# Kernel tuning notes

Hardware: AMD Instinct MI355X
Metric: run time of the kernel (lower is better)

Reference implementation:

```python
import jax, jax.numpy as jnp
import numpy as np

ALPHA = 1.0
EPS = 1e-09
N_PATCH = 128


def _triplet_loss(xp, xn, alpha, eps):
    # xp, xn: [B, N, D], assumed L2-normalized rows
    n = xp.shape[1]
    p_dist = 2.0 - 2.0 * jnp.einsum('bnd,bmd->bnm', xp, xp)   # [B,N,N]
    pn_dist = 2.0 - 2.0 * jnp.einsum('bnd,bmd->bnm', xp, xn)  # [B,N,N]
    # ppn_dist[b,i,j,k] = alpha + p_dist[b,i,j] - pn_dist[b,i,k]
    ppn = alpha + p_dist[:, :, :, None] - pn_dist[:, :, None, :]  # [B,N,N,N]
    mask = ppn <= 0
    pos = jnp.where(mask, 0.0, ppn)
    num = jnp.sum(pos, axis=-1)                                # [B,N,N]
    den = n - jnp.sum(mask, axis=-1).astype(pos.dtype) + eps   # [B,N,N]
    return jnp.mean(num / den)


def setup_inputs() -> dict:
    key = jax.random.key(0)
    latent = jax.random.normal(key, (8192, 512), dtype=jnp.float32)
    return {"latent": latent}


def reference(latent):
    bsz = latent.shape[0] // (2 * N_PATCH)
    latent = latent / jnp.linalg.norm(latent, axis=-1, keepdims=True)
    latent = latent.reshape(bsz, 2, N_PATCH, -1)
    t_latent, c_latent = latent[:, 0], latent[:, 1]
    loss = _triplet_loss(t_latent, c_latent, ALPHA, EPS) + _triplet_loss(c_latent, t_latent, ALPHA, EPS)
    return loss
```

## Files before the change

kernel.cpp:

```cpp
#include <hip/hip_runtime.h>
#include <hip/hip_bf16.h>

constexpr int   D      = 512;
constexpr float ALPHA  = 1.0f;
constexpr float EPS    = 1e-9f;
constexpr float INV_CNT = 1.0f / (32.0f * 128.0f * 128.0f);

constexpr size_t NRM_OFF  = 0;
constexpr size_t PART_OFF = 8388608;

typedef short bf16x8 __attribute__((ext_vector_type(8)));
typedef float f32x4  __attribute__((ext_vector_type(4)));

__device__ __forceinline__ short f2bf(float f) {
    unsigned u = __builtin_bit_cast(unsigned, f);
    unsigned r = (u + 0x7FFFu + ((u >> 16) & 1u)) >> 16;
    return (short)r;
}

typedef __attribute__((address_space(3))) char lds_char;
typedef const __attribute__((address_space(1))) char g_char;
__device__ __forceinline__ void glds16(const void* g, void* l) {
    __builtin_amdgcn_global_load_lds((g_char*)g, (lds_char*)l, 16, 0, 0);
}


__global__ __launch_bounds__(256) void k_normalize(const float* __restrict__ in,
                                                   short* __restrict__ nrm2) {
    const int wid  = threadIdx.x >> 6;
    const int lane = threadIdx.x & 63;
    const int p    = blockIdx.x;
    const int r    = (p & 7) * 1024 + (p >> 3) * 4 + wid;
    const int b    = r >> 8;
    const int row  = r & 255;
    const float4* src = (const float4*)(in + (size_t)r * D);
    float4 x0 = src[2 * lane];
    float4 x1 = src[2 * lane + 1];
    float ss = x0.x*x0.x + x0.y*x0.y + x0.z*x0.z + x0.w*x0.w
             + x1.x*x1.x + x1.y*x1.y + x1.z*x1.z + x1.w*x1.w;
    #pragma unroll
    for (int o = 32; o > 0; o >>= 1) ss += __shfl_xor(ss, o, 64);
    const float inv = rsqrtf(ss);
    bf16x8 v;
    v[0] = f2bf(x0.x * inv); v[1] = f2bf(x0.y * inv);
    v[2] = f2bf(x0.z * inv); v[3] = f2bf(x0.w * inv);
    v[4] = f2bf(x1.x * inv); v[5] = f2bf(x1.y * inv);
    v[6] = f2bf(x1.z * inv); v[7] = f2bf(x1.w * inv);
    const int ks   = lane >> 2;
    const int slot = ((lane & 3) + (row >> 1)) & 3;
    char* dst = (char*)nrm2 + ((((size_t)b * 16 + ks) * 256 + row) * 64 + slot * 16);
    *(bf16x8*)dst = v;
}

constexpr int PSTR = 260;

__global__ __launch_bounds__(256, 4) void k_fused(const short* __restrict__ nrm2,
                                                  float* __restrict__ part) {
    __shared__ __align__(16) char smem[32832];

    const int p     = blockIdx.x;
    const int slot  = p >> 3;
    const int b     = (p & 7) * 4 + (slot & 3);
    const int rem   = slot >> 2;
    const int chunk = rem & 7;
    const int half  = rem >> 3;
    const int w     = threadIdx.x >> 6;
    const int lane  = threadIdx.x & 63;
    const int fr    = lane & 15;
    const int kg    = lane >> 4;

    const char* batchbase = (const char*)nrm2 + (size_t)b * 16 * 256 * 64;

    const int Arow  = half * 128 + chunk * 16 + fr;
    const int sigma = (kg + (fr >> 1)) & 3;
    const char* gA  = batchbase + Arow * 64 + sigma * 16;

    const char* gBl = batchbase + w * 4096 + lane * 16;
    auto stageB = [&](int ks, int bi) {
        const char* s = gBl + (size_t)ks * 16384;
        char* d = &smem[bi * 16384 + w * 4096];
        glds16(s,        d);
        glds16(s + 1024, d + 1024);
        glds16(s + 2048, d + 2048);
        glds16(s + 3072, d + 3072);
    };

    f32x4 acc0 = {0.f,0.f,0.f,0.f}, acc1 = {0.f,0.f,0.f,0.f};
    f32x4 acc2 = {0.f,0.f,0.f,0.f}, acc3 = {0.f,0.f,0.f,0.f};
    bf16x8 aA[2];

    aA[0] = *(const bf16x8*)(gA);
    stageB(0, 0);

    const int ro0 = ( 0 + fr) * 64 + sigma * 16;
    const int ro1 = (16 + fr) * 64 + sigma * 16;
    const int ro2 = (32 + fr) * 64 + sigma * 16;
    const int ro3 = (48 + fr) * 64 + sigma * 16;

    #pragma unroll
    for (int s = 0; s < 16; s++) {
        if (s < 15) {
            aA[(s + 1) & 1] = *(const bf16x8*)(gA + (size_t)(s + 1) * 16384);
            stageB(s + 1, (s + 1) & 1);
            asm volatile("s_waitcnt vmcnt(5)" ::: "memory");
        } else {
            asm volatile("s_waitcnt vmcnt(0)" ::: "memory");
        }
        __builtin_amdgcn_sched_barrier(0);
        const int bo = (s & 1) * 16384 + w * 4096;
        bf16x8 b0 = *(const bf16x8*)&smem[bo + ro0];
        bf16x8 b1 = *(const bf16x8*)&smem[bo + ro1];
        bf16x8 b2 = *(const bf16x8*)&smem[bo + ro2];
        bf16x8 b3 = *(const bf16x8*)&smem[bo + ro3];
        acc0 = __builtin_amdgcn_mfma_f32_16x16x32_bf16(aA[s & 1], b0, acc0, 0, 0, 0);
        acc1 = __builtin_amdgcn_mfma_f32_16x16x32_bf16(aA[s & 1], b1, acc1, 0, 0, 0);
        acc2 = __builtin_amdgcn_mfma_f32_16x16x32_bf16(aA[s & 1], b2, acc2, 0, 0, 0);
        acc3 = __builtin_amdgcn_mfma_f32_16x16x32_bf16(aA[s & 1], b3, acc3, 0, 0, 0);
    }

    __syncthreads();

    float* P   = (float*)smem;
    float* red = (float*)&smem[32768];

    {
        const int rw = kg * 4;
        const int cw = w * 64 + fr;
        #pragma unroll
        for (int q = 0; q < 4; q++) P[(rw + q) * PSTR + cw]      = acc0[q];
        #pragma unroll
        for (int q = 0; q < 4; q++) P[(rw + q) * PSTR + cw + 16] = acc1[q];
        #pragma unroll
        for (int q = 0; q < 4; q++) P[(rw + q) * PSTR + cw + 32] = acc2[q];
        #pragma unroll
        for (int q = 0; q < 4; q++) P[(rw + q) * PSTR + cw + 48] = acc3[q];
    }
    __syncthreads();

    const int pd_off = half ? 128 : 0;
    const int pn_off = 128 - pd_off;
    float wacc = 0.f;
    #pragma unroll
    for (int rr = 0; rr < 4; rr++) {
        const int r = w * 4 + rr;
        float* prow = &P[r * PSTR];

        const float g0 = prow[pd_off + lane];
        const float g1 = prow[pd_off + lane + 64];
        float v0 = prow[pn_off + lane];
        float v1 = prow[pn_off + lane + 64];

        #pragma unroll
        for (int kk = 2; kk <= 128; kk <<= 1) {
            if (kk == 128) {
                const float lo = fminf(v0, v1);
                const float hi = fmaxf(v0, v1);
                v0 = lo; v1 = hi;
            }
            #pragma unroll
            for (int j = (kk == 128 ? 32 : (kk >> 1)); j >= 1; j >>= 1) {
                const float p0 = __shfl_xor(v0, j, 64);
                const float p1 = __shfl_xor(v1, j, 64);
                const bool up0 = (lane & kk) == 0;
                const bool up1 = ((lane + 64) & kk) == 0;
                const bool lower = (lane & j) == 0;
                v0 = (up0 == lower) ? fminf(v0, p0) : fmaxf(v0, p0);
                v1 = (up1 == lower) ? fminf(v1, p1) : fmaxf(v1, p1);
            }
        }

        float inc0 = v0, inc1 = v1;
        #pragma unroll
        for (int o = 1; o < 64; o <<= 1) {
            const float t0 = __shfl_up(inc0, o, 64);
            const float t1 = __shfl_up(inc1, o, 64);
            if (lane >= o) { inc0 += t0; inc1 += t1; }
        }
        const float tot0  = __shfl(inc0, 63, 64);
        const float total = tot0 + __shfl(inc1, 63, 64);

        prow[lane]            = v0;
        prow[64 + lane]       = v1;
        prow[130 + 1 + lane]  = inc0;
        prow[130 + 65 + lane] = tot0 + inc1;
        if (lane == 0) prow[130] = 0.f;

        #pragma unroll
        for (int h = 0; h < 2; h++) {
            const float g   = h ? g1 : g0;
            const float tau = g - 0.5f * ALPHA;
            const float a   = ALPHA - 2.f * g;
            int pos = 0;
            #pragma unroll
            for (int st = 128; st > 0; st >>= 1) {
                const int nidx = pos + st;
                const float sv = prow[nidx - 1];
                pos = ((nidx <= 128) && (sv <= tau)) ? nidx : pos;
            }
            const float cnt = (float)(128 - pos);
            const float pre = prow[130 + pos];
            const float num = cnt * a + 2.f * (total - pre);
            wacc += num / (cnt + EPS);
        }
    }

    #pragma unroll
    for (int o = 32; o > 0; o >>= 1) wacc += __shfl_xor(wacc, o, 64);
    if (lane == 0) red[w] = wacc;
    __syncthreads();
    if (threadIdx.x == 0)
        part[p] = red[0] + red[1] + red[2] + red[3];
}

__global__ __launch_bounds__(512) void k_reduce(const float* __restrict__ part,
                                                float* __restrict__ out) {
    __shared__ float red[8];
    const int w    = threadIdx.x >> 6;
    const int lane = threadIdx.x & 63;
    float s = part[threadIdx.x];
    #pragma unroll
    for (int o = 32; o > 0; o >>= 1) s += __shfl_xor(s, o, 64);
    if (lane == 0) red[w] = s;
    __syncthreads();
    if (threadIdx.x == 0) {
        float t = 0.f;
        #pragma unroll
        for (int i = 0; i < 8; i++) t += red[i];
        out[0] = t * INV_CNT;
    }
}

extern "C" void kernel_launch(void* const* d_in, const int* in_sizes, int n_in,
                              void* d_out, int out_size, void* d_ws, size_t ws_size,
                              hipStream_t stream) {
    const float* latent = (const float*)d_in[0];
    float* out  = (float*)d_out;
    char*  wsb  = (char*)d_ws;
    short* nrm2 = (short*)(wsb + NRM_OFF);
    float* part = (float*)(wsb + PART_OFF);

    hipLaunchKernelGGL(k_normalize, dim3(2048), dim3(256), 0, stream, latent, nrm2);
    hipLaunchKernelGGL(k_fused,     dim3(512),  dim3(256), 0, stream, nrm2, part);
    hipLaunchKernelGGL(k_reduce,    dim3(1),    dim3(512), 0, stream, part, out);
}
```

Measured before the change: 30.33 us.

## Load GEMM B operand directly from global memory instead of LDS staging

Removes the double-buffered global-to-LDS staging of the B operand with its explicit waitcnt pipeline. Each wave now reads its A and B fragments straight from global memory into registers for every k-step. LDS use drops to the space needed for the epilogue, which may allow more resident blocks. In exchange it loses the explicit prefetch overlap and depends on cache hits for B reuse. The __syncthreads before the P writes is also dropped, which is safe only because LDS is no longer written during the GEMM.

```diff
diff --git a/kernel.cpp b/kernel.cpp
--- a/kernel.cpp
+++ b/kernel.cpp
@@ -16,12 +16,6 @@
     unsigned u = __builtin_bit_cast(unsigned, f);
     unsigned r = (u + 0x7FFFu + ((u >> 16) & 1u)) >> 16;
     return (short)r;
-}
-
-typedef __attribute__((address_space(3))) char lds_char;
-typedef const __attribute__((address_space(1))) char g_char;
-__device__ __forceinline__ void glds16(const void* g, void* l) {
-    __builtin_amdgcn_global_load_lds((g_char*)g, (lds_char*)l, 16, 0, 0);
 }
 
 
@@ -56,7 +50,7 @@
 
 __global__ __launch_bounds__(256, 4) void k_fused(const short* __restrict__ nrm2,
                                                   float* __restrict__ part) {
-    __shared__ __align__(16) char smem[32832];
+    __shared__ __align__(16) char smem[16672];
 
     const int p     = blockIdx.x;
     const int slot  = p >> 3;
@@ -71,57 +65,35 @@
 
     const char* batchbase = (const char*)nrm2 + (size_t)b * 16 * 256 * 64;
 
-    const int Arow  = half * 128 + chunk * 16 + fr;
     const int sigma = (kg + (fr >> 1)) & 3;
-    const char* gA  = batchbase + Arow * 64 + sigma * 16;
-
-    const char* gBl = batchbase + w * 4096 + lane * 16;
-    auto stageB = [&](int ks, int bi) {
-        const char* s = gBl + (size_t)ks * 16384;
-        char* d = &smem[bi * 16384 + w * 4096];
-        glds16(s,        d);
-        glds16(s + 1024, d + 1024);
-        glds16(s + 2048, d + 2048);
-        glds16(s + 3072, d + 3072);
-    };
+
+    const int Arow = half * 128 + chunk * 16 + fr;
+    const char* gA = batchbase + Arow * 64 + sigma * 16;
+
+    const char* gB0 = batchbase + (w * 64 +  0 + fr) * 64 + sigma * 16;
+    const char* gB1 = gB0 + 16 * 64;
+    const char* gB2 = gB0 + 32 * 64;
+    const char* gB3 = gB0 + 48 * 64;
 
     f32x4 acc0 = {0.f,0.f,0.f,0.f}, acc1 = {0.f,0.f,0.f,0.f};
     f32x4 acc2 = {0.f,0.f,0.f,0.f}, acc3 = {0.f,0.f,0.f,0.f};
-    bf16x8 aA[2];
-
-    aA[0] = *(const bf16x8*)(gA);
-    stageB(0, 0);
-
-    const int ro0 = ( 0 + fr) * 64 + sigma * 16;
-    const int ro1 = (16 + fr) * 64 + sigma * 16;
-    const int ro2 = (32 + fr) * 64 + sigma * 16;
-    const int ro3 = (48 + fr) * 64 + sigma * 16;
 
     #pragma unroll
     for (int s = 0; s < 16; s++) {
-        if (s < 15) {
-            aA[(s + 1) & 1] = *(const bf16x8*)(gA + (size_t)(s + 1) * 16384);
-            stageB(s + 1, (s + 1) & 1);
-            asm volatile("s_waitcnt vmcnt(5)" ::: "memory");
-        } else {
-            asm volatile("s_waitcnt vmcnt(0)" ::: "memory");
-        }
-        __builtin_amdgcn_sched_barrier(0);
-        const int bo = (s & 1) * 16384 + w * 4096;
-        bf16x8 b0 = *(const bf16x8*)&smem[bo + ro0];
-        bf16x8 b1 = *(const bf16x8*)&smem[bo + ro1];
-        bf16x8 b2 = *(const bf16x8*)&smem[bo + ro2];
-        bf16x8 b3 = *(const bf16x8*)&smem[bo + ro3];
-        acc0 = __builtin_amdgcn_mfma_f32_16x16x32_bf16(aA[s & 1], b0, acc0, 0, 0, 0);
-        acc1 = __builtin_amdgcn_mfma_f32_16x16x32_bf16(aA[s & 1], b1, acc1, 0, 0, 0);
-        acc2 = __builtin_amdgcn_mfma_f32_16x16x32_bf16(aA[s & 1], b2, acc2, 0, 0, 0);
-        acc3 = __builtin_amdgcn_mfma_f32_16x16x32_bf16(aA[s & 1], b3, acc3, 0, 0, 0);
-    }
-
-    __syncthreads();
+        const size_t o = (size_t)s * 16384;
+        const bf16x8 a  = *(const bf16x8*)(gA  + o);
+        const bf16x8 b0 = *(const bf16x8*)(gB0 + o);
+        const bf16x8 b1 = *(const bf16x8*)(gB1 + o);
+        const bf16x8 b2 = *(const bf16x8*)(gB2 + o);
+        const bf16x8 b3 = *(const bf16x8*)(gB3 + o);
+        acc0 = __builtin_amdgcn_mfma_f32_16x16x32_bf16(a, b0, acc0, 0, 0, 0);
+        acc1 = __builtin_amdgcn_mfma_f32_16x16x32_bf16(a, b1, acc1, 0, 0, 0);
+        acc2 = __builtin_amdgcn_mfma_f32_16x16x32_bf16(a, b2, acc2, 0, 0, 0);
+        acc3 = __builtin_amdgcn_mfma_f32_16x16x32_bf16(a, b3, acc3, 0, 0, 0);
+    }
 
     float* P   = (float*)smem;
-    float* red = (float*)&smem[32768];
+    float* red = (float*)&smem[16640];
 
     {
         const int rw = kg * 4;
```

After: 30.52 us. About the same (+0.6%).
